# Kernel tuning notes

Hardware: AMD Instinct MI355X
Metric: run time of the kernel (lower is better)

The kernel has to match this reference:

```python
import jax, jax.numpy as jnp
import numpy as np

NUM_GRAPHS = 256
NEG_SLOPE = 0.2


def _gatv2(x, src, dst, Wl, Wr, att, bias, num_nodes):
    # GATv2Conv (heads=1): e_ij = att . leaky_relu(Wl x_j + Wr x_i), softmax over in-edges of i
    xl = x @ Wl  # [N, H] source transform
    xr = x @ Wr  # [N, H] target transform
    msg = xl[src]                      # [E, H]
    e = jax.nn.leaky_relu(msg + xr[dst], NEG_SLOPE) @ att  # [E]
    # segment softmax over destination node
    e_max = jax.ops.segment_max(e, dst, num_segments=num_nodes)
    e_exp = jnp.exp(e - e_max[dst])
    denom = jax.ops.segment_sum(e_exp, dst, num_segments=num_nodes)
    alpha = e_exp / denom[dst]         # [E]
    out = jax.ops.segment_sum(alpha[:, None] * msg, dst, num_segments=num_nodes)
    return out + bias


def setup_inputs() -> dict:
    key = jax.random.key(0)
    ks = jax.random.split(key, 16)
    N, E, D, H, O = 100000, 1600000, 64, 64, 64
    s = 0.05
    inp = {
        "x": jax.random.normal(ks[0], (N, D), dtype=jnp.float32),
        "edge_index": jax.random.randint(ks[1], (2, E), 0, N, dtype=jnp.int64),
        "batch": jnp.sort(jax.random.randint(ks[2], (N,), 0, NUM_GRAPHS, dtype=jnp.int64)),
        "W1l": jax.random.normal(ks[3], (D, H), dtype=jnp.float32) * s,
        "W1r": jax.random.normal(ks[4], (D, H), dtype=jnp.float32) * s,
        "att1": jax.random.normal(ks[5], (H,), dtype=jnp.float32) * s,
        "b1": jnp.zeros((H,), dtype=jnp.float32),
        "W2": jax.random.normal(ks[6], (H, H), dtype=jnp.float32) * s,
        "att2": jax.random.normal(ks[7], (H,), dtype=jnp.float32) * s,
        "b2": jnp.zeros((H,), dtype=jnp.float32),
        "W3": jax.random.normal(ks[8], (H, H), dtype=jnp.float32) * s,
        "att3": jax.random.normal(ks[9], (H,), dtype=jnp.float32) * s,
        "b3": jnp.zeros((H,), dtype=jnp.float32),
        "Wlin": jax.random.normal(ks[10], (H, O), dtype=jnp.float32) * s,
        "blin": jnp.zeros((O,), dtype=jnp.float32),
    }
    return inp


def reference(x, edge_index, batch, W1l, W1r, att1, b1, W2, att2, b2, W3, att3, b3, Wlin, blin):
    N = x.shape[0]
    # PyG GATv2Conv default add_self_loops=True
    loops = jnp.arange(N, dtype=edge_index.dtype)
    src = jnp.concatenate([edge_index[0], loops])
    dst = jnp.concatenate([edge_index[1], loops])

    h = jax.nn.relu(_gatv2(x, src, dst, W1l, W1r, att1, b1, N))
    h = jax.nn.relu(_gatv2(h, src, dst, W2, W2, att2, b2, N))  # share_weights=True
    h = _gatv2(h, src, dst, W3, W3, att3, b3, N)

    # global mean pool over graphs
    sums = jax.ops.segment_sum(h, batch, num_segments=NUM_GRAPHS)
    cnts = jax.ops.segment_sum(jnp.ones((N,), dtype=h.dtype), batch, num_segments=NUM_GRAPHS)
    pooled = sums / jnp.maximum(cnts, 1.0)[:, None]
    # dropout is identity in eval mode
    return pooled @ Wlin + blin
```

## Files before the change

### kernel.cpp

```cpp
#include <hip/hip_runtime.h>
#include <hip/hip_fp16.h>
#include <math.h>

#define NEG_SLOPE 0.2f
#define NUM_GRAPHS 256
#define LOG2E_F 1.44269504088896f

#define EPB   3328
#define EPT   13
#define BCAP  5120
#define MAXB  392

typedef _Float16 f16x2 __attribute__((ext_vector_type(2)));

__device__ __forceinline__ f16x2 bc16(unsigned u) { return __builtin_bit_cast(f16x2, u); }

__device__ __forceinline__ float hsum16_bcast(float x) {
    x += __int_as_float(__builtin_amdgcn_update_dpp(0, __float_as_int(x), 0x111, 0xF, 0xF, false));
    x += __int_as_float(__builtin_amdgcn_update_dpp(0, __float_as_int(x), 0x112, 0xF, 0xF, false));
    x += __int_as_float(__builtin_amdgcn_update_dpp(0, __float_as_int(x), 0x114, 0xF, 0xF, false));
    x += __int_as_float(__builtin_amdgcn_update_dpp(0, __float_as_int(x), 0x118, 0xF, 0xF, false));
    return __int_as_float(__builtin_amdgcn_ds_swizzle(__float_as_int(x), 0x1F0));
}

__device__ __forceinline__ float score16(f16x2 v0, f16x2 v1, f16x2 x0, f16x2 x1,
                                         f16x2 a0, f16x2 a1) {
    f16x2 t0 = v0 + x0, t1 = v1 + x1;
    t0 = __builtin_elementwise_max(t0, t0 * (_Float16)NEG_SLOPE);
    t1 = __builtin_elementwise_max(t1, t1 * (_Float16)NEG_SLOPE);
#if __has_builtin(__builtin_amdgcn_fdot2)
    return __builtin_amdgcn_fdot2(a1, t1, __builtin_amdgcn_fdot2(a0, t0, 0.0f, false), false);
#else
    return (float)a0.x * (float)t0.x + (float)a0.y * (float)t0.y
         + (float)a1.x * (float)t1.x + (float)a1.y * (float)t1.y;
#endif
}

#define ACC4(V0, V1, W)                      \
    acc0 = fmaf((float)(V0).x, (W), acc0);   \
    acc1 = fmaf((float)(V0).y, (W), acc1);   \
    acc2 = fmaf((float)(V1).x, (W), acc2);   \
    acc3 = fmaf((float)(V1).y, (W), acc3);

#define GATHER(IDX, P)                                                   \
    P[0] = *(const uint2*)(xl + ((size_t)(IDX).x << 6) + 4 * q);         \
    P[1] = *(const uint2*)(xl + ((size_t)(IDX).y << 6) + 4 * q);         \
    P[2] = *(const uint2*)(xl + ((size_t)(IDX).z << 6) + 4 * q);         \
    P[3] = *(const uint2*)(xl + ((size_t)(IDX).w << 6) + 4 * q);

#define COMPUTE(P, C)                                                    \
    _Pragma("unroll")                                                    \
    for (int i_ = 0; i_ < 4; ++i_) {                                     \
        f16x2 V0 = bc16(P[i_].x), V1 = bc16(P[i_].y);                    \
        float p_ = hsum16_bcast(score16(V0, V1, x0, x1, a0, a1));        \
        bool valid_ = (16 * (C) + 4 * i_ + slot) < degs;                 \
        float w_ = valid_ ? exp2f(p_) : 0.f;                             \
        l += w_;                                                         \
        ACC4(V0, V1, w_);                                                \
    }


__device__ __forceinline__ void bucketA_body(char* smem, int bid, int t,
                                             const int* __restrict__ src,
                                             const int* __restrict__ dst,
                                             unsigned* __restrict__ bucketFill,
                                             uint2* __restrict__ bucketArr,
                                             int E, int NBUCK) {
    uint2* sEdge = (uint2*)smem;
    unsigned* hist  = (unsigned*)(smem + EPB * 8);
    unsigned* lscan = hist + MAXB;
    unsigned* ebase = lscan + MAXB;
    unsigned* efill = ebase + MAXB;
    int e0 = bid * EPB;
    int cntE = E - e0; if (cntE > EPB) cntE = EPB;

    for (int b = t; b < MAXB; b += 256) { hist[b] = 0u; efill[b] = 0u; }
    __syncthreads();

    int es[EPT], ed[EPT];
#pragma unroll
    for (int k = 0; k < EPT; ++k) {
        int i = t + k * 256;
        bool v = i < cntE;
        es[k] = v ? src[e0 + i] : 0;
        ed[k] = v ? dst[e0 + i] : -1;
        if (v) atomicAdd(&hist[(unsigned)ed[k] >> 8], 1u);
    }
    __syncthreads();

    if (t < 64) {
        unsigned vals[7]; unsigned tot = 0u;
#pragma unroll
        for (int k = 0; k < 7; ++k) {
            int b = t * 7 + k;
            vals[k] = (b < MAXB) ? hist[b] : 0u;
            tot += vals[k];
        }
        unsigned sc = tot;
#pragma unroll
        for (int off = 1; off < 64; off <<= 1) {
            unsigned n = __shfl_up(sc, off, 64);
            if (t >= off) sc += n;
        }
        unsigned run = sc - tot;
#pragma unroll
        for (int k = 0; k < 7; ++k) {
            int b = t * 7 + k;
            if (b < MAXB) { lscan[b] = run; run += vals[k]; }
        }
    }
    __syncthreads();

    for (int b = t; b < NBUCK; b += 256) {
        unsigned c = hist[b];
        ebase[b] = c ? atomicAdd(&bucketFill[b], c) : 0u;
    }
    __syncthreads();

#pragma unroll
    for (int k = 0; k < EPT; ++k) {
        if (ed[k] >= 0) {
            unsigned b = (unsigned)ed[k] >> 8;
            unsigned p = lscan[b] + atomicAdd(&efill[b], 1u);
            sEdge[p] = make_uint2((unsigned)es[k], (unsigned)ed[k]);
        }
    }
    __syncthreads();

    for (int i = t; i < cntE; i += 256) {
        uint2 e = sEdge[i];
        unsigned b = e.y >> 8;
        unsigned pos = ebase[b] + ((unsigned)i - lscan[b]);
        if (pos < BCAP) bucketArr[(size_t)b * BCAP + pos] = e;
    }
}

__device__ __forceinline__ void gemm_stage(const float* __restrict__ X, float (*sXT)[65],
                                           int r0, int t, int N) {
    int lr = t >> 2;
    int c0s = (t & 3) * 16;
    int row = r0 + lr;
    float4 tmp[4];
    if (row < N) {
        const float4* Xv = (const float4*)(X + (size_t)row * 64 + c0s);
#pragma unroll
        for (int i = 0; i < 4; ++i) tmp[i] = Xv[i];
    } else {
#pragma unroll
        for (int i = 0; i < 4; ++i) tmp[i] = make_float4(0.f, 0.f, 0.f, 0.f);
    }
#pragma unroll
    for (int i = 0; i < 4; ++i) {
        sXT[c0s + i*4 + 0][lr] = tmp[i].x;
        sXT[c0s + i*4 + 1][lr] = tmp[i].y;
        sXT[c0s + i*4 + 2][lr] = tmp[i].z;
        sXT[c0s + i*4 + 3][lr] = tmp[i].w;
    }
    __syncthreads();
}

__device__ __forceinline__ void store16_f16(__half* Y16, int orow, int cbase, const float* acc) {
    __half2 h8[8];
#pragma unroll
    for (int c = 0; c < 8; ++c) h8[c] = __floats2half2_rn(acc[2*c], acc[2*c+1]);
    uint4* d16 = (uint4*)(Y16 + (size_t)orow * 64 + cbase);
    d16[0] = ((uint4*)h8)[0];
    d16[1] = ((uint4*)h8)[1];
}

__global__ __launch_bounds__(256) void k_gemm1_bucketA(
        const float* __restrict__ X, const float* __restrict__ Wl, const float* __restrict__ Wr,
        __half* __restrict__ Yl16, __half* __restrict__ Yr16, int N,
        const int* __restrict__ src, const int* __restrict__ dst,
        unsigned* __restrict__ bucketFill, uint2* __restrict__ bucketArr,
        int E, int NBUCK, int aBlocks) {
    __shared__ uint4 smemq[2056];
    char* smem = (char*)smemq;
    int bid = blockIdx.x;
    int t = threadIdx.x;
    if (bid < aBlocks) {
        bucketA_body(smem, bid, t, src, dst, bucketFill, bucketArr, E, NBUCK);
        return;
    }
    float (*sXT)[65] = (float(*)[65])smem;
    int r0 = (bid - aBlocks) * 64;
    gemm_stage(X, sXT, r0, t, N);
    int lane = t & 63;
    int cbase = __builtin_amdgcn_readfirstlane((t >> 6) * 16);
    int orow = r0 + lane;
    float accl[16], accr[16];
#pragma unroll
    for (int c = 0; c < 16; ++c) { accl[c] = 0.f; accr[c] = 0.f; }
    for (int k = 0; k < 64; ++k) {
        float xk = sXT[k][lane];
        const float* wl = Wl + k * 64 + cbase;
        const float* wr = Wr + k * 64 + cbase;
#pragma unroll
        for (int c = 0; c < 16; ++c) { accl[c] += xk * wl[c]; accr[c] += xk * wr[c]; }
    }
    if (orow < N) {
        store16_f16(Yl16, orow, cbase, accl);
        store16_f16(Yr16, orow, cbase, accr);
    }
}

__global__ __launch_bounds__(256) void k_bucketB(const uint2* __restrict__ bucketArr,
                                                 const unsigned* __restrict__ bucketFill,
                                                 int* __restrict__ cnt, int* __restrict__ csrF,
                                                 const int* __restrict__ batch,
                                                 int* __restrict__ gstart,
                                                 int N, int E) {
    __shared__ int stage[256 * 64];
    __shared__ unsigned h[256];
    int t = threadIdx.x;
    int b = blockIdx.x;
    int n0 = b << 8;
    h[t] = 0u;
    {
        uint4* sz = (uint4*)stage;
        for (int k = t; k < 256 * 16; k += 256) sz[k] = make_uint4(0u, 0u, 0u, 0u);
    }
    __syncthreads();

    unsigned ec = bucketFill[b]; if (ec > BCAP) ec = BCAP;
    for (unsigned i = t; i < ec; i += 256) {
        uint2 e = bucketArr[(size_t)b * BCAP + i];
        unsigned v = e.y & 255u;
        unsigned r = atomicAdd(&h[v], 1u);
        if (r < 64u) stage[(v << 6) + ((r & 3u) << 4) + (r >> 2)] = (int)e.x;
    }
    __syncthreads();

    int node = n0 + t;
    if (node < N) {
        unsigned d = h[t];
        cnt[node] = (int)(d < 64u ? d : 64u);
        int bb = batch[node];
        if (node == 0) {
            for (int g = 0; g <= bb; ++g) gstart[g] = 0;
        } else {
            int pb = batch[node - 1];
            for (int g = pb + 1; g <= bb; ++g) gstart[g] = node;
        }
        if (node == N - 1) {
            for (int g = bb + 1; g <= NUM_GRAPHS; ++g) gstart[g] = N;
        }
    }

    int nrows = N - n0; if (nrows > 256) nrows = 256;
    int total4 = nrows << 4;
    uint4* d4 = (uint4*)(csrF + ((size_t)n0 << 6));
    const uint4* s4 = (const uint4*)stage;
    for (int k = t; k < total4; k += 256) d4[k] = s4[k];
}

__global__ void k_gemm_l2(const float* __restrict__ X, const float* __restrict__ W,
                          __half* __restrict__ Y16, int N) {
    __shared__ float sXT[64][65];
    int t = threadIdx.x;
    int r0 = blockIdx.x * 64;
    gemm_stage(X, sXT, r0, t, N);
    int lane = t & 63;
    int cbase = __builtin_amdgcn_readfirstlane((t >> 6) * 16);
    int orow = r0 + lane;
    float acc[16];
#pragma unroll
    for (int c = 0; c < 16; ++c) acc[c] = 0.f;
    for (int k = 0; k < 64; ++k) {
        float xk = sXT[k][lane];
        const float* wp = W + k * 64 + cbase;
#pragma unroll
        for (int c = 0; c < 16; ++c) acc[c] += xk * wp[c];
    }
    if (orow < N) {
        store16_f16(Y16, orow, cbase, acc);
    }
}


__global__ void k_agg16(const __half* __restrict__ xl, const __half* __restrict__ xrh,
                        const float* __restrict__ att, const float* __restrict__ bias,
                        const int* __restrict__ cnt, const int* __restrict__ csrF,
                        float* __restrict__ out, int N, int do_relu) {
    int wid = (blockIdx.x * blockDim.x + threadIdx.x) >> 6;
    if (wid >= N) return;
    int lane = threadIdx.x & 63;
    int q = lane & 15, slot = lane >> 4;

    uint2 ux = *(const uint2*)(xrh + ((size_t)wid << 6) + 4 * q);
    uint2 us = *(const uint2*)(xl  + ((size_t)wid << 6) + 4 * q);
    float4 at4 = *(const float4*)(att + 4 * q);

    int degs = __builtin_amdgcn_readfirstlane(cnt[wid]);
    const int* myidx = csrF + ((size_t)wid << 6) + slot * 16;
    uint4 i0 = *(const uint4*)myidx;
    uint4 i1 = *(const uint4*)(myidx + 4);

    uint2 A[4], Bv[4];
    GATHER(i0, A);
    if (degs > 16) { GATHER(i1, Bv); }

    f16x2 x0 = bc16(ux.x), x1 = bc16(ux.y);
    f16x2 a0 = {(_Float16)(at4.x * LOG2E_F), (_Float16)(at4.y * LOG2E_F)};
    f16x2 a1 = {(_Float16)(at4.z * LOG2E_F), (_Float16)(at4.w * LOG2E_F)};

    f16x2 s0 = bc16(us.x), s1 = bc16(us.y);
    float ps = hsum16_bcast(score16(s0, s1, x0, x1, a0, a1));
    float wsf = (slot == 0) ? exp2f(ps) : 0.f;
    float l = wsf;
    float acc0 = (float)s0.x * wsf, acc1 = (float)s0.y * wsf;
    float acc2 = (float)s1.x * wsf, acc3 = (float)s1.y * wsf;

    COMPUTE(A, 0);
    if (degs > 16) {
        if (degs > 32) { uint4 i2 = *(const uint4*)(myidx + 8); GATHER(i2, A); }
        COMPUTE(Bv, 1);
        if (degs > 32) {
            uint4 i3;
            if (degs > 48) { i3 = *(const uint4*)(myidx + 12); GATHER(i3, Bv); }
            COMPUTE(A, 2);
            if (degs > 48) { COMPUTE(Bv, 3); }
        }
    }

#pragma unroll
    for (int o = 16; o <= 32; o <<= 1) {
        l += __shfl_xor(l, o, 64);
        acc0 += __shfl_xor(acc0, o, 64);
        acc1 += __shfl_xor(acc1, o, 64);
        acc2 += __shfl_xor(acc2, o, 64);
        acc3 += __shfl_xor(acc3, o, 64);
    }
    if (slot == 0) {
        float rl = 1.0f / l;
        float4 bv = *(const float4*)(bias + 4 * q);
        float o0 = acc0 * rl + bv.x;
        float o1 = acc1 * rl + bv.y;
        float o2 = acc2 * rl + bv.z;
        float o3 = acc3 * rl + bv.w;
        if (do_relu) {
            o0 = fmaxf(o0, 0.f); o1 = fmaxf(o1, 0.f);
            o2 = fmaxf(o2, 0.f); o3 = fmaxf(o3, 0.f);
        }
        *(float4*)(out + (size_t)wid * 64 + 4 * q) = make_float4(o0, o1, o2, o3);
    }
}


__global__ void k_pool_final(const float* __restrict__ h, const int* __restrict__ gstart,
                             const float* __restrict__ Wlin, const float* __restrict__ blin,
                             float* __restrict__ out) {
    int wave = (blockIdx.x * blockDim.x + threadIdx.x) >> 6;
    int lane = threadIdx.x & 63;
    if (wave >= NUM_GRAPHS) return;
    int g = wave;
    int i0 = gstart[g], i1 = gstart[g + 1];
    float s0 = 0.f, s1 = 0.f, s2 = 0.f, s3 = 0.f;
    int i = i0;
    for (; i + 4 <= i1; i += 4) {
        s0 += h[(size_t)i * 64 + lane];
        s1 += h[(size_t)(i + 1) * 64 + lane];
        s2 += h[(size_t)(i + 2) * 64 + lane];
        s3 += h[(size_t)(i + 3) * 64 + lane];
    }
    for (; i < i1; ++i) s0 += h[(size_t)i * 64 + lane];
    float s = (s0 + s1) + (s2 + s3);
    float c = (float)((i1 - i0) > 1 ? (i1 - i0) : 1);
    float pld = s / c;
    float acc = blin[lane];
    for (int k = 0; k < 64; ++k) {
        acc += __shfl(pld, k, 64) * Wlin[k * 64 + lane];
    }
    out[g * 64 + lane] = acc;
}


extern "C" void kernel_launch(void* const* d_in, const int* in_sizes, int n_in,
                              void* d_out, int out_size, void* d_ws, size_t ws_size,
                              hipStream_t stream) {
    const float* x    = (const float*)d_in[0];
    const int*   ei   = (const int*)d_in[1];
    const int*   batch= (const int*)d_in[2];
    const float* W1l  = (const float*)d_in[3];
    const float* W1r  = (const float*)d_in[4];
    const float* att1 = (const float*)d_in[5];
    const float* b1   = (const float*)d_in[6];
    const float* W2   = (const float*)d_in[7];
    const float* att2 = (const float*)d_in[8];
    const float* b2   = (const float*)d_in[9];
    const float* W3   = (const float*)d_in[10];
    const float* att3 = (const float*)d_in[11];
    const float* b3   = (const float*)d_in[12];
    const float* Wlin = (const float*)d_in[13];
    const float* blin = (const float*)d_in[14];

    const int N = in_sizes[0] / 64;
    const int E = in_sizes[1] / 2;
    const int* src = ei;
    const int* dst = ei + E;
    const int NBUCK = (N + 255) >> 8;

    char* p = (char*)d_ws;
    auto alloc = [&](size_t bytes) -> void* {
        void* r = (void*)p;
        p += (bytes + 255) & ~(size_t)255;
        return r;
    };
    float*  bufB32 = (float*)alloc((size_t)N * 64 * 4);
    __half* buf16  = (__half*)alloc((size_t)N * 64 * 2);
    __half* bufC16 = (__half*)alloc((size_t)N * 64 * 2);
    int*    csrF   = (int*)alloc((size_t)N * 64 * 4);
    int*    cnt    = (int*)alloc((size_t)N * 4);
    int*    gstart = (int*)alloc((size_t)(NUM_GRAPHS + 1) * 4);
    uint2*    bucketArr  = (uint2*)bufB32;
    unsigned* bucketFill = (unsigned*)((char*)bufB32 + ((size_t)20 << 20));

    const int B = 256;
    const int gemmBlocks = (N + 63) / 64;
    const int aggBlocks = ((size_t)N * 64 + B - 1) / B;
    const int aBlocks = (E + EPB - 1) / EPB;

    hipMemsetAsync(bucketFill, 0, (size_t)NBUCK * 4, stream);
    k_gemm1_bucketA<<<aBlocks + gemmBlocks, B, 0, stream>>>(
        x, W1l, W1r, buf16, bufC16, N, src, dst, bucketFill, bucketArr, E, NBUCK, aBlocks);
    k_bucketB<<<NBUCK, B, 0, stream>>>(bucketArr, bucketFill, cnt, csrF, batch, gstart, N, E);

    k_agg16<<<aggBlocks, B, 0, stream>>>(buf16, bufC16, att1, b1, cnt, csrF, bufB32, N, 1);

    k_gemm_l2<<<gemmBlocks, B, 0, stream>>>(bufB32, W2, buf16, N);
    k_agg16<<<aggBlocks, B, 0, stream>>>(buf16, buf16, att2, b2, cnt, csrF, bufB32, N, 1);

    k_gemm_l2<<<gemmBlocks, B, 0, stream>>>(bufB32, W3, buf16, N);
    k_agg16<<<aggBlocks, B, 0, stream>>>(buf16, buf16, att3, b3, cnt, csrF, bufB32, N, 0);

    k_pool_final<<<(NUM_GRAPHS * 64 + B - 1) / B, B, 0, stream>>>(bufB32, gstart, Wlin, blin, (float*)d_out);
}
```

Baseline: 354.5 us.

## Compute attention scores with MFMA and fold self-loop into CSR slot

The edge-aggregation kernel now has each lane handle one edge of a 16-edge chunk with 8-wide fp16 vectors. The per-edge attention dot products are computed with two 16x16x32 fp16 MFMA instructions instead of fdot2 plus per-edge DPP reductions. The self-loop is stored as the first CSR entry during bucketing, which removes the separate self-edge path. CSR layout becomes contiguous, and the attention vectors are pre-scaled by log2e and converted to fp16 once in an extra block of the first kernel. The trade-off is 16 accumulators per lane that must be DPP-reduced at the end, more register pressure, and self-loops now consuming one of the 64 neighbor slots.

```diff
diff --git a/kernel.cpp b/kernel.cpp
--- a/kernel.cpp
+++ b/kernel.cpp
@@ -11,9 +11,10 @@
 #define BCAP  5120
 #define MAXB  392
 
-typedef _Float16 f16x2 __attribute__((ext_vector_type(2)));
-
-__device__ __forceinline__ f16x2 bc16(unsigned u) { return __builtin_bit_cast(f16x2, u); }
+typedef _Float16 half8 __attribute__((ext_vector_type(8)));
+typedef float f32x4 __attribute__((ext_vector_type(4)));
+
+__device__ __forceinline__ half8 bch8(uint4 u) { return __builtin_bit_cast(half8, u); }
 
 __device__ __forceinline__ float hsum16_bcast(float x) {
     x += __int_as_float(__builtin_amdgcn_update_dpp(0, __float_as_int(x), 0x111, 0xF, 0xF, false));
@@ -22,42 +23,6 @@
     x += __int_as_float(__builtin_amdgcn_update_dpp(0, __float_as_int(x), 0x118, 0xF, 0xF, false));
     return __int_as_float(__builtin_amdgcn_ds_swizzle(__float_as_int(x), 0x1F0));
 }
-
-__device__ __forceinline__ float score16(f16x2 v0, f16x2 v1, f16x2 x0, f16x2 x1,
-                                         f16x2 a0, f16x2 a1) {
-    f16x2 t0 = v0 + x0, t1 = v1 + x1;
-    t0 = __builtin_elementwise_max(t0, t0 * (_Float16)NEG_SLOPE);
-    t1 = __builtin_elementwise_max(t1, t1 * (_Float16)NEG_SLOPE);
-#if __has_builtin(__builtin_amdgcn_fdot2)
-    return __builtin_amdgcn_fdot2(a1, t1, __builtin_amdgcn_fdot2(a0, t0, 0.0f, false), false);
-#else
-    return (float)a0.x * (float)t0.x + (float)a0.y * (float)t0.y
-         + (float)a1.x * (float)t1.x + (float)a1.y * (float)t1.y;
-#endif
-}
-
-#define ACC4(V0, V1, W)                      \
-    acc0 = fmaf((float)(V0).x, (W), acc0);   \
-    acc1 = fmaf((float)(V0).y, (W), acc1);   \
-    acc2 = fmaf((float)(V1).x, (W), acc2);   \
-    acc3 = fmaf((float)(V1).y, (W), acc3);
-
-#define GATHER(IDX, P)                                                   \
-    P[0] = *(const uint2*)(xl + ((size_t)(IDX).x << 6) + 4 * q);         \
-    P[1] = *(const uint2*)(xl + ((size_t)(IDX).y << 6) + 4 * q);         \
-    P[2] = *(const uint2*)(xl + ((size_t)(IDX).z << 6) + 4 * q);         \
-    P[3] = *(const uint2*)(xl + ((size_t)(IDX).w << 6) + 4 * q);
-
-#define COMPUTE(P, C)                                                    \
-    _Pragma("unroll")                                                    \
-    for (int i_ = 0; i_ < 4; ++i_) {                                     \
-        f16x2 V0 = bc16(P[i_].x), V1 = bc16(P[i_].y);                    \
-        float p_ = hsum16_bcast(score16(V0, V1, x0, x1, a0, a1));        \
-        bool valid_ = (16 * (C) + 4 * i_ + slot) < degs;                 \
-        float w_ = valid_ ? exp2f(p_) : 0.f;                             \
-        l += w_;                                                         \
-        ACC4(V0, V1, w_);                                                \
-    }
 
 
 __device__ __forceinline__ void bucketA_body(char* smem, int bid, int t,
@@ -173,13 +138,23 @@
         __half* __restrict__ Yl16, __half* __restrict__ Yr16, int N,
         const int* __restrict__ src, const int* __restrict__ dst,
         unsigned* __restrict__ bucketFill, uint2* __restrict__ bucketArr,
-        int E, int NBUCK, int aBlocks) {
+        int E, int NBUCK, int aBlocks, int gemmBlocks,
+        const float* __restrict__ att1, const float* __restrict__ att2,
+        const float* __restrict__ att3, __half* __restrict__ att16) {
     __shared__ uint4 smemq[2056];
     char* smem = (char*)smemq;
     int bid = blockIdx.x;
     int t = threadIdx.x;
     if (bid < aBlocks) {
         bucketA_body(smem, bid, t, src, dst, bucketFill, bucketArr, E, NBUCK);
+        return;
+    }
+    if (bid >= aBlocks + gemmBlocks) {
+        if (t < 192) {
+            int layer = t >> 6, f = t & 63;
+            const float* ap = (layer == 0) ? att1 : (layer == 1) ? att2 : att3;
+            att16[layer * 64 + f] = __float2half(ap[f] * LOG2E_F);
+        }
         return;
     }
     float (*sXT)[65] = (float(*)[65])smem;
@@ -215,11 +190,13 @@
     int t = threadIdx.x;
     int b = blockIdx.x;
     int n0 = b << 8;
-    h[t] = 0u;
+    h[t] = 1u;
     {
         uint4* sz = (uint4*)stage;
         for (int k = t; k < 256 * 16; k += 256) sz[k] = make_uint4(0u, 0u, 0u, 0u);
     }
+    __syncthreads();
+    stage[t << 6] = n0 + t;
     __syncthreads();
 
     unsigned ec = bucketFill[b]; if (ec > BCAP) ec = BCAP;
@@ -227,7 +204,7 @@
         uint2 e = bucketArr[(size_t)b * BCAP + i];
         unsigned v = e.y & 255u;
         unsigned r = atomicAdd(&h[v], 1u);
-        if (r < 64u) stage[(v << 6) + ((r & 3u) << 4) + (r >> 2)] = (int)e.x;
+        if (r < 64u) stage[(v << 6) + r] = (int)e.x;
     }
     __syncthreads();
 
@@ -278,71 +255,89 @@
 }
 
 
+#define AGG_GATHER(P0, P1, C)                                              \
+    { int i_ = crow[(C) * 16 + c];                                         \
+      const __half* vr_ = xl + ((size_t)i_ << 6) + fbase;                  \
+      P0 = *(const uint4*)vr_; P1 = *(const uint4*)(vr_ + 32); }
+
+#define AGG_CHUNK(P0, P1, C)                                               \
+    { half8 v0 = bch8(P0), v1 = bch8(P1);                                  \
+      half8 t0 = v0 + X0, t1 = v1 + X1;                                    \
+      t0 = __builtin_elementwise_max(t0, t0 * (_Float16)NEG_SLOPE);        \
+      t1 = __builtin_elementwise_max(t1, t1 * (_Float16)NEG_SLOPE);        \
+      f32x4 d = __builtin_amdgcn_mfma_f32_16x16x32_f16(A0, t0, (f32x4){0.f,0.f,0.f,0.f}, 0, 0, 0); \
+      d = __builtin_amdgcn_mfma_f32_16x16x32_f16(A1, t1, d, 0, 0, 0);      \
+      float w = ((C) * 16 + c < degs) ? exp2f(d[0]) : 0.f;                 \
+      l_acc += w;                                                          \
+      _Pragma("unroll") for (int j_ = 0; j_ < 8; ++j_) {                   \
+          acc[j_]     = fmaf((float)v0[j_], w, acc[j_]);                   \
+          acc[8 + j_] = fmaf((float)v1[j_], w, acc[8 + j_]);               \
+      } }
+
 __global__ void k_agg16(const __half* __restrict__ xl, const __half* __restrict__ xrh,
-                        const float* __restrict__ att, const float* __restrict__ bias,
+                        const __half* __restrict__ att16, const float* __restrict__ bias,
                         const int* __restrict__ cnt, const int* __restrict__ csrF,
                         float* __restrict__ out, int N, int do_relu) {
     int wid = (blockIdx.x * blockDim.x + threadIdx.x) >> 6;
     if (wid >= N) return;
     int lane = threadIdx.x & 63;
-    int q = lane & 15, slot = lane >> 4;
-
-    uint2 ux = *(const uint2*)(xrh + ((size_t)wid << 6) + 4 * q);
-    uint2 us = *(const uint2*)(xl  + ((size_t)wid << 6) + 4 * q);
-    float4 at4 = *(const float4*)(att + 4 * q);
+    int c = lane & 15, g = lane >> 4;
+    int fbase = g * 8;
 
     int degs = __builtin_amdgcn_readfirstlane(cnt[wid]);
-    const int* myidx = csrF + ((size_t)wid << 6) + slot * 16;
-    uint4 i0 = *(const uint4*)myidx;
-    uint4 i1 = *(const uint4*)(myidx + 4);
-
-    uint2 A[4], Bv[4];
-    GATHER(i0, A);
-    if (degs > 16) { GATHER(i1, Bv); }
-
-    f16x2 x0 = bc16(ux.x), x1 = bc16(ux.y);
-    f16x2 a0 = {(_Float16)(at4.x * LOG2E_F), (_Float16)(at4.y * LOG2E_F)};
-    f16x2 a1 = {(_Float16)(at4.z * LOG2E_F), (_Float16)(at4.w * LOG2E_F)};
-
-    f16x2 s0 = bc16(us.x), s1 = bc16(us.y);
-    float ps = hsum16_bcast(score16(s0, s1, x0, x1, a0, a1));
-    float wsf = (slot == 0) ? exp2f(ps) : 0.f;
-    float l = wsf;
-    float acc0 = (float)s0.x * wsf, acc1 = (float)s0.y * wsf;
-    float acc2 = (float)s1.x * wsf, acc3 = (float)s1.y * wsf;
-
-    COMPUTE(A, 0);
+    const int* crow = csrF + ((size_t)wid << 6);
+
+    const __half* xrrow = xrh + ((size_t)wid << 6);
+    uint4 ux0 = *(const uint4*)(xrrow + fbase);
+    uint4 ux1 = *(const uint4*)(xrrow + 32 + fbase);
+    uint4 ua0 = *(const uint4*)(att16 + fbase);
+    uint4 ua1 = *(const uint4*)(att16 + 32 + fbase);
+
+    uint4 pa0, pa1, pb0, pb1;
+    AGG_GATHER(pa0, pa1, 0);
+    if (degs > 16) AGG_GATHER(pb0, pb1, 1);
+
+    half8 X0 = bch8(ux0), X1 = bch8(ux1);
+    half8 A0 = bch8(ua0), A1 = bch8(ua1);
+
+    float l_acc = 0.f;
+    float acc[16];
+#pragma unroll
+    for (int j = 0; j < 16; ++j) acc[j] = 0.f;
+
+    AGG_CHUNK(pa0, pa1, 0);
     if (degs > 16) {
-        if (degs > 32) { uint4 i2 = *(const uint4*)(myidx + 8); GATHER(i2, A); }
-        COMPUTE(Bv, 1);
+        if (degs > 32) AGG_GATHER(pa0, pa1, 2);
+        AGG_CHUNK(pb0, pb1, 1);
         if (degs > 32) {
-            uint4 i3;
-            if (degs > 48) { i3 = *(const uint4*)(myidx + 12); GATHER(i3, Bv); }
-            COMPUTE(A, 2);
-            if (degs > 48) { COMPUTE(Bv, 3); }
-        }
-    }
-
-#pragma unroll
-    for (int o = 16; o <= 32; o <<= 1) {
-        l += __shfl_xor(l, o, 64);
-        acc0 += __shfl_xor(acc0, o, 64);
-        acc1 += __shfl_xor(acc1, o, 64);
-        acc2 += __shfl_xor(acc2, o, 64);
-        acc3 += __shfl_xor(acc3, o, 64);
-    }
-    if (slot == 0) {
-        float rl = 1.0f / l;
-        float4 bv = *(const float4*)(bias + 4 * q);
-        float o0 = acc0 * rl + bv.x;
-        float o1 = acc1 * rl + bv.y;
-        float o2 = acc2 * rl + bv.z;
-        float o3 = acc3 * rl + bv.w;
+            if (degs > 48) AGG_GATHER(pb0, pb1, 3);
+            AGG_CHUNK(pa0, pa1, 2);
+            if (degs > 48) AGG_CHUNK(pb0, pb1, 3);
+        }
+    }
+
+#pragma unroll
+    for (int j = 0; j < 16; ++j) acc[j] = hsum16_bcast(acc[j]);
+    l_acc = hsum16_bcast(l_acc);
+
+    if (g == ((c & 7) >> 1)) {
+        float rl = 1.0f / l_acc;
+        float4 bv = *(const float4*)(bias + 4 * c);
+        float4 o;
+        if (c < 8) {
+            if ((c & 1) == 0) o = make_float4(acc[0], acc[1], acc[2], acc[3]);
+            else              o = make_float4(acc[4], acc[5], acc[6], acc[7]);
+        } else {
+            if ((c & 1) == 0) o = make_float4(acc[8], acc[9], acc[10], acc[11]);
+            else              o = make_float4(acc[12], acc[13], acc[14], acc[15]);
+        }
+        o.x = o.x * rl + bv.x; o.y = o.y * rl + bv.y;
+        o.z = o.z * rl + bv.z; o.w = o.w * rl + bv.w;
         if (do_relu) {
-            o0 = fmaxf(o0, 0.f); o1 = fmaxf(o1, 0.f);
-            o2 = fmaxf(o2, 0.f); o3 = fmaxf(o3, 0.f);
-        }
-        *(float4*)(out + (size_t)wid * 64 + 4 * q) = make_float4(o0, o1, o2, o3);
+            o.x = fmaxf(o.x, 0.f); o.y = fmaxf(o.y, 0.f);
+            o.z = fmaxf(o.z, 0.f); o.w = fmaxf(o.w, 0.f);
+        }
+        *(float4*)(out + (size_t)wid * 64 + 4 * c) = o;
     }
 }
 
@@ -365,8 +360,8 @@
     }
     for (; i < i1; ++i) s0 += h[(size_t)i * 64 + lane];
     float s = (s0 + s1) + (s2 + s3);
-    float c = (float)((i1 - i0) > 1 ? (i1 - i0) : 1);
-    float pld = s / c;
+    float cden = (float)((i1 - i0) > 1 ? (i1 - i0) : 1);
+    float pld = s / cden;
     float acc = blin[lane];
     for (int k = 0; k < 64; ++k) {
         acc += __shfl(pld, k, 64) * Wlin[k * 64 + lane];
@@ -412,6 +407,7 @@
     int*    csrF   = (int*)alloc((size_t)N * 64 * 4);
     int*    cnt    = (int*)alloc((size_t)N * 4);
     int*    gstart = (int*)alloc((size_t)(NUM_GRAPHS + 1) * 4);
+    __half* att16  = (__half*)alloc((size_t)3 * 64 * 2);
     uint2*    bucketArr  = (uint2*)bufB32;
     unsigned* bucketFill = (unsigned*)((char*)bufB32 + ((size_t)20 << 20));
 
@@ -421,17 +417,18 @@
     const int aBlocks = (E + EPB - 1) / EPB;
 
     hipMemsetAsync(bucketFill, 0, (size_t)NBUCK * 4, stream);
-    k_gemm1_bucketA<<<aBlocks + gemmBlocks, B, 0, stream>>>(
-        x, W1l, W1r, buf16, bufC16, N, src, dst, bucketFill, bucketArr, E, NBUCK, aBlocks);
+    k_gemm1_bucketA<<<aBlocks + gemmBlocks + 1, B, 0, stream>>>(
+        x, W1l, W1r, buf16, bufC16, N, src, dst, bucketFill, bucketArr,
+        E, NBUCK, aBlocks, gemmBlocks, att1, att2, att3, att16);
     k_bucketB<<<NBUCK, B, 0, stream>>>(bucketArr, bucketFill, cnt, csrF, batch, gstart, N, E);
 
-    k_agg16<<<aggBlocks, B, 0, stream>>>(buf16, bufC16, att1, b1, cnt, csrF, bufB32, N, 1);
+    k_agg16<<<aggBlocks, B, 0, stream>>>(buf16, bufC16, att16, b1, cnt, csrF, bufB32, N, 1);
 
     k_gemm_l2<<<gemmBlocks, B, 0, stream>>>(bufB32, W2, buf16, N);
-    k_agg16<<<aggBlocks, B, 0, stream>>>(buf16, buf16, att2, b2, cnt, csrF, bufB32, N, 1);
+    k_agg16<<<aggBlocks, B, 0, stream>>>(buf16, buf16, att16 + 64, b2, cnt, csrF, bufB32, N, 1);
 
     k_gemm_l2<<<gemmBlocks, B, 0, stream>>>(bufB32, W3, buf16, N);
-    k_agg16<<<aggBlocks, B, 0, stream>>>(buf16, buf16, att3, b3, cnt, csrF, bufB32, N, 0);
+    k_agg16<<<aggBlocks, B, 0, stream>>>(buf16, buf16, att16 + 128, b3, cnt, csrF, bufB32, N, 0);
 
     k_pool_final<<<(NUM_GRAPHS * 64 + B - 1) / B, B, 0, stream>>>(bufB32, gstart, Wlin, blin, (float*)d_out);
 }
```

New measurement: 373.8 us. 5.4% more time.
